# Kernel tuning notes

Measured on AMD Instinct MI355X. Metric: run time of the kernel, lower is better.

Reference implementation:

```python
import jax, jax.numpy as jnp
import numpy as np
import math

EPS = 1e-6
NUM_HEADS = 8


def _layernorm(x, g, b):
    mu = jnp.mean(x, axis=-1, keepdims=True)
    var = jnp.mean(jnp.square(x - mu), axis=-1, keepdims=True)
    return (x - mu) * jax.lax.rsqrt(var + EPS) * g + b


def _pos_embed(n, d):
    pos = jnp.arange(n, dtype=jnp.float32)[:, None]                  # [N,1]
    div = jnp.exp(jnp.arange(0, d, 2, dtype=jnp.float32) * (-math.log(10000.0) / d))
    ang = pos * div                                                  # [N,d/2]
    pe = jnp.stack([jnp.sin(ang), jnp.cos(ang)], axis=-1).reshape(n, d)
    return pe


def setup_inputs() -> dict:
    key = jax.random.key(0)
    B, N, C, L = 2, 2048, 256, 4
    ks = jax.random.split(key, 6)
    s = 0.02
    return {
        "x": jax.random.normal(ks[0], (B, N, C), jnp.float32),
        "qkv_w": jax.random.normal(ks[1], (L, C, 3 * C), jnp.float32) * s,
        "proj_w": jax.random.normal(ks[2], (L, C, C), jnp.float32) * s,
        "proj_b": jnp.zeros((L, C), jnp.float32),
        "w1": jax.random.normal(ks[3], (L, C, C), jnp.float32) * s,
        "b1": jnp.zeros((L, C), jnp.float32),
        "w2": jax.random.normal(ks[4], (L, C, C), jnp.float32) * s,
        "b2": jnp.zeros((L, C), jnp.float32),
        "g1": jnp.ones((L, C), jnp.float32),
        "be1": jnp.zeros((L, C), jnp.float32),
        "g2": jnp.ones((L, C), jnp.float32),
        "be2": jnp.zeros((L, C), jnp.float32),
    }


def reference(x, qkv_w, proj_w, proj_b, w1, b1, w2, b2, g1, be1, g2, be2):
    B, N, C = x.shape
    L = qkv_w.shape[0]
    H = NUM_HEADS
    dh = C // H
    scale = dh ** -0.5

    x = x + _pos_embed(N, C)[None]

    for l in range(L):
        # --- attention (manual QKV, post-norm residual as in source) ---
        qkv = (x @ qkv_w[l]).reshape(B, N, 3, H, dh)
        q, k, v = qkv[:, :, 0], qkv[:, :, 1], qkv[:, :, 2]           # [B,N,H,dh]
        attn = jnp.einsum('bqhd,bkhd->bhqk', q, k) * scale           # [B,H,N,N]
        attn = jax.nn.softmax(attn, axis=-1)
        o = jnp.einsum('bhqk,bkhd->bqhd', attn, v).reshape(B, N, C)
        o = o @ proj_w[l] + proj_b[l]
        x = _layernorm(x + o, g1[l], be1[l])
        # --- MLP (GELU exact, as torch nn.GELU default) ---
        m = jax.nn.gelu(x @ w1[l] + b1[l], approximate=False) @ w2[l] + b2[l]
        x = _layernorm(x + m, g2[l], be2[l])
    return x
```

## Files before the change

### kernel.cpp

```cpp
#include <hip/hip_runtime.h>
#include <math.h>

#define Bd 2
#define Nd 2048
#define Cd 256
#define Ld 4
#define Hd 8
#define Md (Bd*Nd)
#define BHd 16
#define U32d 1024
#define SPLITd 4

typedef __attribute__((ext_vector_type(8))) short bf16x8;
typedef __attribute__((ext_vector_type(4))) float f32x4;
typedef __attribute__((ext_vector_type(16))) float f32x16;
typedef __attribute__((ext_vector_type(4))) short shortx4;

static __device__ inline f32x4 mfma16(bf16x8 a, bf16x8 b, f32x4 c) {
    return __builtin_amdgcn_mfma_f32_16x16x32_bf16(a, b, c, 0, 0, 0);
}
static __device__ inline f32x16 mfma32(bf16x8 a, bf16x8 b, f32x16 c) {
    return __builtin_amdgcn_mfma_f32_32x32x16_bf16(a, b, c, 0, 0, 0);
}
static __device__ inline short f2bf(float f) {
    union { float f; unsigned u; } v; v.f = f;
    unsigned r = (v.u + 0x7fff + ((v.u >> 16) & 1)) >> 16;
    return (short)r;
}
static __device__ inline unsigned pkbf(float a, float b) {
    unsigned r;
    asm("v_cvt_pk_bf16_f32 %0, %1, %2" : "=v"(r) : "v"(a), "v"(b));
    return r;
}
static __device__ inline float bf2f(unsigned u) {
    return __uint_as_float((u & 0xffffu) << 16);
}

__global__ __launch_bounds__(256)
void prep_kernel(const float* __restrict__ x_in, const float* __restrict__ qkv_w,
                 const float* __restrict__ proj_w, const float* __restrict__ w1,
                 const float* __restrict__ w2, float* __restrict__ xf,
                 short* __restrict__ xb, short* __restrict__ qkvT,
                 short* __restrict__ projT, short* __restrict__ w1T,
                 short* __restrict__ w2T, float qscale)
{
    __shared__ float tile[32][33];
    int id = blockIdx.x;
    if (id < 1536) {
        const float* src; short* dst; int Nc; float scale; int lim; int rem; int l;
        if (id < 768)       { l = id / 192;         rem = id % 192; src = qkv_w;  dst = qkvT;  Nc = 768; scale = qscale; lim = 256; }
        else if (id < 1024) { l = (id - 768) / 64;  rem = (id - 768) % 64;  src = proj_w; dst = projT; Nc = 256; scale = 1.f; lim = 0; }
        else if (id < 1280) { l = (id - 1024) / 64; rem = (id - 1024) % 64; src = w1;     dst = w1T;   Nc = 256; scale = 1.f; lim = 0; }
        else                { l = (id - 1280) / 64; rem = (id - 1280) % 64; src = w2;     dst = w2T;   Nc = 256; scale = 1.f; lim = 0; }
        int nb = Nc >> 5;
        int c0 = (rem % nb) * 32, k0 = (rem / nb) * 32;
        src += (size_t)l * 256 * Nc;
        dst += (size_t)l * Nc * 256;
        int tx = threadIdx.x & 31, ty = threadIdx.x >> 5;
#pragma unroll
        for (int i = 0; i < 4; i++) {
            int k = ty + 8 * i;
            tile[k][tx] = src[(size_t)(k0 + k) * Nc + c0 + tx];
        }
        __syncthreads();
#pragma unroll
        for (int i = 0; i < 4; i++) {
            int cc = ty + 8 * i;
            int col = c0 + cc;
            float v = tile[tx][cc];
            if (col < lim) v *= scale;
            dst[(size_t)col * 256 + k0 + tx] = f2bf(v);
        }
    } else {
        int i = (id - 1536) * 256 + threadIdx.x;
        int c = i & (Cd - 1);
        int n = (i >> 8) & (Nd - 1);
        const float kneg = -9.210340371976184f / 256.0f;
        float div = __expf((float)(c & ~1) * kneg);
        float ang = (float)n * div;
        float pe = (c & 1) ? cosf(ang) : sinf(ang);
        float v = x_in[i] + pe;
        xf[i] = v;
        xb[i] = f2bf(v);
    }
}

__global__ __launch_bounds__(256)
void qkv_gemm_kernel(const short* __restrict__ Ab, const short* __restrict__ WT,
                     short* __restrict__ Qb, short* __restrict__ Kb,
                     short* __restrict__ Vtb)
{
    int t = threadIdx.x, w = t >> 6, l = t & 63, c = l & 15, g = l >> 4;
    int rowBase = blockIdx.y * 128 + w * 32;
    int colBase = blockIdx.x * 32;
    const f32x4 zero = {0.f, 0.f, 0.f, 0.f};
    f32x4 acc[2][2] = {{zero, zero}, {zero, zero}};
    const short* ap0 = Ab + (size_t)(rowBase + c) * 256 + g * 8;
    const short* ap1 = ap0 + 16 * 256;
    const short* bp0 = WT + (size_t)(colBase + c) * 256 + g * 8;
    const short* bp1 = bp0 + 16 * 256;
#pragma unroll
    for (int kc = 0; kc < 256; kc += 32) {
        bf16x8 a0 = *(const bf16x8*)(ap0 + kc);
        bf16x8 a1 = *(const bf16x8*)(ap1 + kc);
        bf16x8 b0 = *(const bf16x8*)(bp0 + kc);
        bf16x8 b1 = *(const bf16x8*)(bp1 + kc);
        acc[0][0] = mfma16(a0, b0, acc[0][0]);
        acc[0][1] = mfma16(a0, b1, acc[0][1]);
        acc[1][0] = mfma16(a1, b0, acc[1][0]);
        acc[1][1] = mfma16(a1, b1, acc[1][1]);
    }
    int region = colBase >> 8;
    if (region < 2) {
        short* dst = (region == 0) ? Qb : Kb;
        int cb = colBase - region * 256;
#pragma unroll
        for (int m = 0; m < 2; m++)
#pragma unroll
            for (int n = 0; n < 2; n++)
#pragma unroll
                for (int r = 0; r < 4; r++)
                    dst[(size_t)(rowBase + 16 * m + 4 * g + r) * 256 + cb + 16 * n + c]
                        = f2bf(acc[m][n][r]);
    } else {
        int b = rowBase >> 11;
        int ntok0 = (rowBase & (Nd - 1)) + 4 * g;
#pragma unroll
        for (int m = 0; m < 2; m++)
#pragma unroll
            for (int n = 0; n < 2; n++) {
                int chg = colBase - 512 + 16 * n + c;
                shortx4 pkv;
#pragma unroll
                for (int r = 0; r < 4; r++) pkv[r] = f2bf(acc[m][n][r]);
                *(shortx4*)&Vtb[(size_t)((b * Hd + (chg >> 5)) * 32 + (chg & 31)) * Nd
                                + ntok0 + 16 * m] = pkv;
            }
    }
}

__global__ __launch_bounds__(256)
void attn_part_kernel(const short* __restrict__ Qb, const short* __restrict__ Kb,
                      const short* __restrict__ Vtb, unsigned* __restrict__ OPb,
                      float* __restrict__ Lsum)
{
    int t = threadIdx.x, w = t >> 6, l = t & 63;
    int l5 = l >> 5, q32 = l & 31;
    int qt = blockIdx.x * 4 + w;
    int bh = blockIdx.y, part = blockIdx.z;
    int b = bh >> 3, h = bh & 7;

    bf16x8 qf0, qf1;
    {
        const short* qp = Qb + ((size_t)(b * Nd + qt * 32 + q32)) * 256 + h * 32 + 8 * l5;
        qf0 = *(const bf16x8*)qp;
        qf1 = *(const bf16x8*)(qp + 16);
    }
    const short* kp = Kb + (size_t)b * Nd * 256 + h * 32 + 8 * l5;
    const short* vp = Vtb + (size_t)(bh * 32 + q32) * Nd + 8 * l5;

    f32x16 O;
#pragma unroll
    for (int i = 0; i < 16; i++) O[i] = 0.f;
    float lsum = 0.f;

    const int kstart = part * (Nd / SPLITd);
    const int kend = (part + 1) * (Nd / SPLITd);

    bf16x8 kf[2][2], vv[4];
#pragma unroll
    for (int sb = 0; sb < 2; sb++)
#pragma unroll
        for (int ks = 0; ks < 2; ks++)
            kf[sb][ks] = *(const bf16x8*)(kp + (size_t)(kstart + 32 * sb + q32) * 256 + 16 * ks);
#pragma unroll
    for (int kc = 0; kc < 4; kc++)
        vv[kc] = *(const bf16x8*)(vp + kstart + 16 * kc);

    for (int k0 = kstart; k0 < kend; k0 += 64) {
        bool has_next = (k0 + 64) < kend;
        bf16x8 kfn[2][2], vvn[4];
        if (has_next) {
            int kn = k0 + 64;
#pragma unroll
            for (int sb = 0; sb < 2; sb++)
#pragma unroll
                for (int ks = 0; ks < 2; ks++)
                    kfn[sb][ks] = *(const bf16x8*)(kp + (size_t)(kn + 32 * sb + q32) * 256 + 16 * ks);
#pragma unroll
            for (int kc = 0; kc < 4; kc++)
                vvn[kc] = *(const bf16x8*)(vp + kn + 16 * kc);
        }

#pragma unroll
        for (int sb = 0; sb < 2; sb++) {
            f32x16 s;
#pragma unroll
            for (int i = 0; i < 16; i++) s[i] = 0.f;
            s = mfma32(kf[sb][0], qf0, s);
            s = mfma32(kf[sb][1], qf1, s);
            float ps = 0.f;
#pragma unroll
            for (int i = 0; i < 16; i++) { s[i] = exp2f(s[i]); ps += s[i]; }
            lsum += ps;
            unsigned wd[8];
#pragma unroll
            for (int i = 0; i < 8; i++) wd[i] = pkbf(s[2 * i], s[2 * i + 1]);
#pragma unroll
            for (int half = 0; half < 2; half++) {
                unsigned a0 = wd[4 * half], a1 = wd[4 * half + 1];
                unsigned b0 = wd[4 * half + 2], b1 = wd[4 * half + 3];
                asm("v_permlane32_swap_b32 %0, %1" : "+v"(a0), "+v"(b0));
                asm("v_permlane32_swap_b32 %0, %1" : "+v"(a1), "+v"(b1));
                union { unsigned u[4]; bf16x8 v; } pa;
                pa.u[0] = a0; pa.u[1] = a1; pa.u[2] = b0; pa.u[3] = b1;
                O = mfma32(pa.v, vv[2 * sb + half], O);
            }
        }
        if (has_next) {
#pragma unroll
            for (int sb = 0; sb < 2; sb++)
#pragma unroll
                for (int ks = 0; ks < 2; ks++) kf[sb][ks] = kfn[sb][ks];
#pragma unroll
            for (int kc = 0; kc < 4; kc++) vv[kc] = vvn[kc];
        }
    }

    lsum += __shfl_xor(lsum, 32, 64);

    int u = bh * 64 + qt;
    unsigned* opb = OPb + ((size_t)part * U32d + u) * 512;
#pragma unroll
    for (int i = 0; i < 16; i += 2) {
        int q = (i & 3) + 8 * (i >> 2) + 4 * l5;
        opb[(q >> 1) * 32 + q32] = pkbf(O[i], O[i + 1]);
    }
    if (l5 == 0) Lsum[((size_t)part * U32d + u) * 32 + q32] = lsum;
}

__global__ __launch_bounds__(512)
void proj_ln_kernel(const unsigned* __restrict__ OPb, const float* __restrict__ Lsum,
                    const short* __restrict__ WT, const float* __restrict__ bias,
                    const float* __restrict__ resid, const float* __restrict__ gg,
                    const float* __restrict__ be, float* __restrict__ outf,
                    short* __restrict__ outb)
{
    __shared__ short Atile[16 * 264];
    __shared__ float red[8][16][2];
    int t = threadIdx.x;
    int rowBase = blockIdx.x * 16;

    {
        int r = t >> 5, seg = t & 31;
        int grow = rowBase + r;
        int bb = grow >> 11;
        int qt = (grow & (Nd - 1)) >> 5;
        int q = grow & 31;
        int h = seg >> 2;
        int dh0 = (seg & 3) * 8;
        int u = (bb * Hd + h) * 64 + qt;
        int sh = (q & 1) * 16;
        float o[8] = {0.f, 0.f, 0.f, 0.f, 0.f, 0.f, 0.f, 0.f};
        float L = 0.f;
#pragma unroll
        for (int p = 0; p < SPLITd; p++) {
            const unsigned* src = OPb + ((size_t)p * U32d + u) * 512 + (q >> 1) * 32 + dh0;
            uint4 w0 = *(const uint4*)src;
            uint4 w1 = *(const uint4*)(src + 4);
            o[0] += bf2f(w0.x >> sh); o[1] += bf2f(w0.y >> sh);
            o[2] += bf2f(w0.z >> sh); o[3] += bf2f(w0.w >> sh);
            o[4] += bf2f(w1.x >> sh); o[5] += bf2f(w1.y >> sh);
            o[6] += bf2f(w1.z >> sh); o[7] += bf2f(w1.w >> sh);
            L += Lsum[((size_t)p * U32d + u) * 32 + q];
        }
        float inv = 1.f / L;
        bf16x8 pk;
#pragma unroll
        for (int j = 0; j < 8; j++) pk[j] = f2bf(o[j] * inv);
        *(bf16x8*)&Atile[r * 264 + seg * 8] = pk;
    }
    __syncthreads();

    int w = t >> 6, l = t & 63, c = l & 15, g = l >> 4;
    const f32x4 zero = {0.f, 0.f, 0.f, 0.f};
    f32x4 acc0 = zero, acc1 = zero;
    const short* bp0 = WT + (size_t)(w * 32 + c) * 256 + g * 8;
    const short* bp1 = bp0 + 16 * 256;
#pragma unroll
    for (int kc = 0; kc < 256; kc += 32) {
        bf16x8 a = *(const bf16x8*)&Atile[c * 264 + g * 8 + kc];
        acc0 = mfma16(a, *(const bf16x8*)(bp0 + kc), acc0);
        acc1 = mfma16(a, *(const bf16x8*)(bp1 + kc), acc1);
    }

    float vv[2][4], s_[4] = {0.f, 0.f, 0.f, 0.f}, sq_[4] = {0.f, 0.f, 0.f, 0.f};
    int col0 = w * 32 + c, col1 = col0 + 16;
    float bi0 = bias[col0], bi1 = bias[col1];
#pragma unroll
    for (int r = 0; r < 4; r++) {
        int row = rowBase + 4 * g + r;
        float v0 = acc0[r] + bi0 + resid[(size_t)row * 256 + col0];
        float v1 = acc1[r] + bi1 + resid[(size_t)row * 256 + col1];
        vv[0][r] = v0; vv[1][r] = v1;
        s_[r] += v0 + v1; sq_[r] += v0 * v0 + v1 * v1;
    }
#pragma unroll
    for (int off = 1; off <= 8; off <<= 1)
#pragma unroll
        for (int r = 0; r < 4; r++) {
            s_[r] += __shfl_xor(s_[r], off, 64);
            sq_[r] += __shfl_xor(sq_[r], off, 64);
        }
    if (c == 0)
#pragma unroll
        for (int r = 0; r < 4; r++) {
            red[w][4 * g + r][0] = s_[r];
            red[w][4 * g + r][1] = sq_[r];
        }
    __syncthreads();
    float mu[4], rs[4];
#pragma unroll
    for (int r = 0; r < 4; r++) {
        float S = 0.f, Q = 0.f;
#pragma unroll
        for (int ww = 0; ww < 8; ww++) { S += red[ww][4 * g + r][0]; Q += red[ww][4 * g + r][1]; }
        mu[r] = S * (1.f / 256.f);
        rs[r] = rsqrtf(Q * (1.f / 256.f) - mu[r] * mu[r] + 1e-6f);
    }
    float gv0 = gg[col0], bv0 = be[col0], gv1 = gg[col1], bv1 = be[col1];
#pragma unroll
    for (int r = 0; r < 4; r++) {
        int row = rowBase + 4 * g + r;
        float o0 = (vv[0][r] - mu[r]) * rs[r] * gv0 + bv0;
        float o1 = (vv[1][r] - mu[r]) * rs[r] * gv1 + bv1;
        outf[(size_t)row * 256 + col0] = o0;
        outf[(size_t)row * 256 + col1] = o1;
        outb[(size_t)row * 256 + col0] = f2bf(o0);
        outb[(size_t)row * 256 + col1] = f2bf(o1);
    }
}

template<int LAST>
__global__ __launch_bounds__(512)
void mlp_kernel(const short* __restrict__ xbin, const short* __restrict__ W1T,
                const float* __restrict__ b1, const short* __restrict__ W2T,
                const float* __restrict__ b2, const float* __restrict__ resid,
                const float* __restrict__ gg, const float* __restrict__ be,
                float* __restrict__ outf, short* __restrict__ outb)
{
    __shared__ short A1[16 * 264];
    __shared__ short A2[16 * 264];
    __shared__ float red[8][16][2];
    int t = threadIdx.x;
    int rowBase = blockIdx.x * 16;

    {
        int r = t >> 5, seg = t & 31;
        *(bf16x8*)&A1[r * 264 + seg * 8] =
            *(const bf16x8*)(xbin + (size_t)(rowBase + r) * 256 + seg * 8);
    }
    __syncthreads();

    int w = t >> 6, l = t & 63, c = l & 15, g = l >> 4;
    const f32x4 zero = {0.f, 0.f, 0.f, 0.f};
    int col0 = w * 32 + c, col1 = col0 + 16;

    {
        f32x4 acc0 = zero, acc1 = zero;
        const short* bp0 = W1T + (size_t)(w * 32 + c) * 256 + g * 8;
        const short* bp1 = bp0 + 16 * 256;
#pragma unroll
        for (int kc = 0; kc < 256; kc += 32) {
            bf16x8 a = *(const bf16x8*)&A1[c * 264 + g * 8 + kc];
            acc0 = mfma16(a, *(const bf16x8*)(bp0 + kc), acc0);
            acc1 = mfma16(a, *(const bf16x8*)(bp1 + kc), acc1);
        }
        float bi0 = b1[col0], bi1 = b1[col1];
#pragma unroll
        for (int r = 0; r < 4; r++) {
            float v0 = acc0[r] + bi0, v1 = acc1[r] + bi1;
            v0 = 0.5f * v0 * (1.f + erff(v0 * 0.7071067811865476f));
            v1 = 0.5f * v1 * (1.f + erff(v1 * 0.7071067811865476f));
            A2[(4 * g + r) * 264 + col0] = f2bf(v0);
            A2[(4 * g + r) * 264 + col1] = f2bf(v1);
        }
    }
    __syncthreads();

    f32x4 acc0 = zero, acc1 = zero;
    const short* bp0 = W2T + (size_t)(w * 32 + c) * 256 + g * 8;
    const short* bp1 = bp0 + 16 * 256;
#pragma unroll
    for (int kc = 0; kc < 256; kc += 32) {
        bf16x8 a = *(const bf16x8*)&A2[c * 264 + g * 8 + kc];
        acc0 = mfma16(a, *(const bf16x8*)(bp0 + kc), acc0);
        acc1 = mfma16(a, *(const bf16x8*)(bp1 + kc), acc1);
    }
    float vv[2][4], s_[4] = {0.f, 0.f, 0.f, 0.f}, sq_[4] = {0.f, 0.f, 0.f, 0.f};
    float bi0 = b2[col0], bi1 = b2[col1];
#pragma unroll
    for (int r = 0; r < 4; r++) {
        int row = rowBase + 4 * g + r;
        float v0 = acc0[r] + bi0 + resid[(size_t)row * 256 + col0];
        float v1 = acc1[r] + bi1 + resid[(size_t)row * 256 + col1];
        vv[0][r] = v0; vv[1][r] = v1;
        s_[r] += v0 + v1; sq_[r] += v0 * v0 + v1 * v1;
    }
#pragma unroll
    for (int off = 1; off <= 8; off <<= 1)
#pragma unroll
        for (int r = 0; r < 4; r++) {
            s_[r] += __shfl_xor(s_[r], off, 64);
            sq_[r] += __shfl_xor(sq_[r], off, 64);
        }
    if (c == 0)
#pragma unroll
        for (int r = 0; r < 4; r++) {
            red[w][4 * g + r][0] = s_[r];
            red[w][4 * g + r][1] = sq_[r];
        }
    __syncthreads();
    float mu[4], rs[4];
#pragma unroll
    for (int r = 0; r < 4; r++) {
        float S = 0.f, Q = 0.f;
#pragma unroll
        for (int ww = 0; ww < 8; ww++) { S += red[ww][4 * g + r][0]; Q += red[ww][4 * g + r][1]; }
        mu[r] = S * (1.f / 256.f);
        rs[r] = rsqrtf(Q * (1.f / 256.f) - mu[r] * mu[r] + 1e-6f);
    }
    float gv0 = gg[col0], bv0 = be[col0], gv1 = gg[col1], bv1 = be[col1];
#pragma unroll
    for (int r = 0; r < 4; r++) {
        int row = rowBase + 4 * g + r;
        float o0 = (vv[0][r] - mu[r]) * rs[r] * gv0 + bv0;
        float o1 = (vv[1][r] - mu[r]) * rs[r] * gv1 + bv1;
        outf[(size_t)row * 256 + col0] = o0;
        outf[(size_t)row * 256 + col1] = o1;
        if (!LAST) {
            outb[(size_t)row * 256 + col0] = f2bf(o0);
            outb[(size_t)row * 256 + col1] = f2bf(o1);
        }
    }
}

extern "C" void kernel_launch(void* const* d_in, const int* in_sizes, int n_in,
                              void* d_out, int out_size, void* d_ws, size_t ws_size,
                              hipStream_t stream)
{
    const float* x_in   = (const float*)d_in[0];
    const float* qkv_w  = (const float*)d_in[1];
    const float* proj_w = (const float*)d_in[2];
    const float* proj_b = (const float*)d_in[3];
    const float* w1     = (const float*)d_in[4];
    const float* b1     = (const float*)d_in[5];
    const float* w2     = (const float*)d_in[6];
    const float* b2     = (const float*)d_in[7];
    const float* g1     = (const float*)d_in[8];
    const float* be1    = (const float*)d_in[9];
    const float* g2     = (const float*)d_in[10];
    const float* be2    = (const float*)d_in[11];
    float* outp = (float*)d_out;

    char* p = (char*)d_ws;
    float* xf    = (float*)p;    p += (size_t)Md * Cd * 4;
    short* xb    = (short*)p;    p += (size_t)Md * Cd * 2;
    short* Qb    = (short*)p;    p += (size_t)Md * Cd * 2;
    short* Kb    = (short*)p;    p += (size_t)Md * Cd * 2;
    short* Vtb   = (short*)p;    p += (size_t)Md * Cd * 2;
    unsigned* OPb = (unsigned*)p; p += (size_t)SPLITd * U32d * 512 * 4;
    float* Lsum  = (float*)p;    p += (size_t)SPLITd * U32d * 32 * 4;
    short* qkvT  = (short*)p;    p += (size_t)Ld * 768 * 256 * 2;
    short* projT = (short*)p;    p += (size_t)Ld * 256 * 256 * 2;
    short* w1T   = (short*)p;    p += (size_t)Ld * 256 * 256 * 2;
    short* w2T   = (short*)p;    p += (size_t)Ld * 256 * 256 * 2;

    const float QSCALE = 0.17677669529663687f * 1.4426950408889634f;
    prep_kernel<<<1536 + Md * Cd / 256, 256, 0, stream>>>(
        x_in, qkv_w, proj_w, w1, w2, xf, xb, qkvT, projT, w1T, w2T, QSCALE);

    for (int l = 0; l < Ld; l++) {
        qkv_gemm_kernel<<<dim3(24, 32), 256, 0, stream>>>(
            xb, qkvT + (size_t)l * 768 * 256, Qb, Kb, Vtb);
        attn_part_kernel<<<dim3(16, BHd, SPLITd), 256, 0, stream>>>(Qb, Kb, Vtb, OPb, Lsum);
        proj_ln_kernel<<<Md / 16, 512, 0, stream>>>(
            OPb, Lsum, projT + (size_t)l * 65536, proj_b + l * 256, xf,
            g1 + l * 256, be1 + l * 256, xf, xb);
        if (l == Ld - 1)
            mlp_kernel<1><<<Md / 16, 512, 0, stream>>>(
                xb, w1T + (size_t)l * 65536, b1 + l * 256,
                w2T + (size_t)l * 65536, b2 + l * 256, xf,
                g2 + l * 256, be2 + l * 256, outp, nullptr);
        else
            mlp_kernel<0><<<Md / 16, 512, 0, stream>>>(
                xb, w1T + (size_t)l * 65536, b1 + l * 256,
                w2T + (size_t)l * 65536, b2 + l * 256, xf,
                g2 + l * 256, be2 + l * 256, xf, xb);
    }
}
```

Measured before the change: 374.5 us.

## Remap attention blocks to XCDs for K/V L2 locality and simplify addressing

The attention kernel now launches as a flat 1D grid and remaps block ids so that the blocks sharing one (part, head) key/value slice land on the same XCD, which should improve L2 reuse of K and V. It also replaces the per-iteration recomputed K/V addresses with incrementing pointers and turns the exp-sum into a pairwise tree reduction to shorten the dependency chain. The mapping assumes round-robin dispatch of blocks across 8 XCDs, and the tree changes floating-point summation order slightly.

```diff
diff --git a/kernel.cpp b/kernel.cpp
--- a/kernel.cpp
+++ b/kernel.cpp
@@ -146,8 +146,11 @@
 {
     int t = threadIdx.x, w = t >> 6, l = t & 63;
     int l5 = l >> 5, q32 = l & 31;
-    int qt = blockIdx.x * 4 + w;
-    int bh = blockIdx.y, part = blockIdx.z;
+    int bid = blockIdx.x;
+    int xcd = bid & 7, j = bid >> 3;
+    int grp = xcd * 8 + (j >> 4);
+    int qt = (j & 15) * 4 + w;
+    int part = grp >> 4, bh = grp & 15;
     int b = bh >> 3, h = bh & 7;
 
     bf16x8 qf0, qf1;
@@ -156,40 +159,41 @@
         qf0 = *(const bf16x8*)qp;
         qf1 = *(const bf16x8*)(qp + 16);
     }
-    const short* kp = Kb + (size_t)b * Nd * 256 + h * 32 + 8 * l5;
-    const short* vp = Vtb + (size_t)(bh * 32 + q32) * Nd + 8 * l5;
+    const int kstart = part * (Nd / SPLITd);
+    const short* kb = Kb + (size_t)b * Nd * 256 + h * 32 + 8 * l5
+                      + (size_t)(kstart + q32) * 256;
+    const short* vb = Vtb + (size_t)(bh * 32 + q32) * Nd + 8 * l5 + kstart;
 
     f32x16 O;
 #pragma unroll
     for (int i = 0; i < 16; i++) O[i] = 0.f;
     float lsum = 0.f;
 
-    const int kstart = part * (Nd / SPLITd);
-    const int kend = (part + 1) * (Nd / SPLITd);
-
     bf16x8 kf[2][2], vv[4];
 #pragma unroll
     for (int sb = 0; sb < 2; sb++)
 #pragma unroll
         for (int ks = 0; ks < 2; ks++)
-            kf[sb][ks] = *(const bf16x8*)(kp + (size_t)(kstart + 32 * sb + q32) * 256 + 16 * ks);
+            kf[sb][ks] = *(const bf16x8*)(kb + sb * 32 * 256 + ks * 16);
 #pragma unroll
     for (int kc = 0; kc < 4; kc++)
-        vv[kc] = *(const bf16x8*)(vp + kstart + 16 * kc);
-
-    for (int k0 = kstart; k0 < kend; k0 += 64) {
-        bool has_next = (k0 + 64) < kend;
+        vv[kc] = *(const bf16x8*)(vb + 16 * kc);
+
+    const int NT = (Nd / SPLITd) / 64;
+    for (int it = 0; it < NT; ++it) {
+        bool has_next = (it + 1) < NT;
         bf16x8 kfn[2][2], vvn[4];
         if (has_next) {
-            int kn = k0 + 64;
+            const short* kn = kb + 64 * 256;
+            const short* vn = vb + 64;
 #pragma unroll
             for (int sb = 0; sb < 2; sb++)
 #pragma unroll
                 for (int ks = 0; ks < 2; ks++)
-                    kfn[sb][ks] = *(const bf16x8*)(kp + (size_t)(kn + 32 * sb + q32) * 256 + 16 * ks);
+                    kfn[sb][ks] = *(const bf16x8*)(kn + sb * 32 * 256 + ks * 16);
 #pragma unroll
             for (int kc = 0; kc < 4; kc++)
-                vvn[kc] = *(const bf16x8*)(vp + kn + 16 * kc);
+                vvn[kc] = *(const bf16x8*)(vn + 16 * kc);
         }
 
 #pragma unroll
@@ -199,13 +203,19 @@
             for (int i = 0; i < 16; i++) s[i] = 0.f;
             s = mfma32(kf[sb][0], qf0, s);
             s = mfma32(kf[sb][1], qf1, s);
-            float ps = 0.f;
-#pragma unroll
-            for (int i = 0; i < 16; i++) { s[i] = exp2f(s[i]); ps += s[i]; }
-            lsum += ps;
+            float e[16];
+#pragma unroll
+            for (int i = 0; i < 16; i++) e[i] = exp2f(s[i]);
+            float p0 = e[0] + e[1],  p1 = e[2] + e[3];
+            float p2 = e[4] + e[5],  p3 = e[6] + e[7];
+            float p4 = e[8] + e[9],  p5 = e[10] + e[11];
+            float p6 = e[12] + e[13], p7 = e[14] + e[15];
+            p0 += p1; p2 += p3; p4 += p5; p6 += p7;
+            p0 += p2; p4 += p6;
+            lsum += p0 + p4;
             unsigned wd[8];
 #pragma unroll
-            for (int i = 0; i < 8; i++) wd[i] = pkbf(s[2 * i], s[2 * i + 1]);
+            for (int i = 0; i < 8; i++) wd[i] = pkbf(e[2 * i], e[2 * i + 1]);
 #pragma unroll
             for (int half = 0; half < 2; half++) {
                 unsigned a0 = wd[4 * half], a1 = wd[4 * half + 1];
@@ -217,6 +227,8 @@
                 O = mfma32(pa.v, vv[2 * sb + half], O);
             }
         }
+        kb += 64 * 256;
+        vb += 64;
         if (has_next) {
 #pragma unroll
             for (int sb = 0; sb < 2; sb++)
@@ -483,7 +495,7 @@
     for (int l = 0; l < Ld; l++) {
         qkv_gemm_kernel<<<dim3(24, 32), 256, 0, stream>>>(
             xb, qkvT + (size_t)l * 768 * 256, Qb, Kb, Vtb);
-        attn_part_kernel<<<dim3(16, BHd, SPLITd), 256, 0, stream>>>(Qb, Kb, Vtb, OPb, Lsum);
+        attn_part_kernel<<<1024, 256, 0, stream>>>(Qb, Kb, Vtb, OPb, Lsum);
         proj_ln_kernel<<<Md / 16, 512, 0, stream>>>(
             OPb, Lsum, projT + (size_t)l * 65536, proj_b + l * 256, xf,
             g1 + l * 256, be1 + l * 256, xf, xb);
```

New measurement: 379.0 us. No clear change (+1.2%).
